# Kernel tuning notes

Hardware: AMD Instinct MI355X
Metric: run time of the kernel (lower is better)

## Reference

```python
import jax, jax.numpy as jnp
import numpy as np

FLOW_W, RECON_W, CONS_W, BIT_W = 1.0, 0.1, 0.1, 0.5
EPS = 1e-7  # guard for log in BCE (torch clamps log at -100)


def setup_inputs() -> dict:
    key = jax.random.key(0)
    k1, k2, k3, k4, k5, k6 = jax.random.split(key, 6)
    B, K, C, T, NB = 8, 4, 2, 262144, 64
    return {
        "separated": jax.random.normal(k1, (B, K, C, T), jnp.float32),
        "sources": jax.random.normal(k2, (B, K, C, T), jnp.float32),
        "mixture": jax.random.normal(k3, (B, C, T), jnp.float32),
        "pred_bits": jax.random.uniform(k4, (B, K, NB), jnp.float32),
        "flow_loss": jax.random.uniform(k5, (1,), jnp.float32),
        "target_bits": jax.random.randint(k6, (B, K, NB), 0, 2, jnp.int32),
    }


def _pit_loss(pred, target):
    # pred/target: [B, K, C, T]; K > 2 path: per-batch KxK MSE cost + greedy matching
    B, K, C, T = pred.shape
    n = C * T
    # cost[b,i,j] = mean((pred[b,i]-target[b,j])^2) expanded to avoid [B,K,K,C,T] intermediate
    p2 = jnp.mean(pred * pred, axis=(-2, -1))            # [B, K]
    t2 = jnp.mean(target * target, axis=(-2, -1))        # [B, K]
    cross = jnp.einsum("bict,bjct->bij", pred, target) / n  # [B, K, K]
    cost = p2[:, :, None] + t2[:, None, :] - 2.0 * cross  # [B, K, K]

    def greedy(c):  # c: [K, K] -> scalar greedy assignment cost
        used = jnp.zeros((K,), bool)
        tot = jnp.zeros((), c.dtype)
        for i in range(K):  # K is small and static
            row = jnp.where(used, jnp.inf, c[i])
            j = jnp.argmin(row)
            tot = tot + row[j]
            used = used.at[j].set(True)
        return tot

    return jnp.mean(jax.vmap(greedy)(cost))  # average over batch


def reference(separated, sources, mixture, pred_bits, flow_loss, target_bits):
    flow = flow_loss[0] * FLOW_W
    recon = _pit_loss(separated, sources) * RECON_W
    mix_hat = separated.sum(axis=1)  # [B, C, T]
    cons = jnp.mean((mix_hat - mixture) ** 2) * CONS_W
    tb = target_bits.astype(pred_bits.dtype)
    p = jnp.clip(pred_bits, EPS, 1.0 - EPS)
    bce = -jnp.mean(tb * jnp.log(p) + (1.0 - tb) * jnp.log(1.0 - p))
    bit = bce * BIT_W
    total = flow + recon + cons + bit
    # [flow_loss, reconstruction_loss, consistency_loss, bit_loss, total_loss]
    return jnp.stack([flow, recon, cons, bit, total])
```

## Files before the change

kernel.cpp:

```cpp
#include <hip/hip_runtime.h>
#include <math.h>

#define BB 8
#define KK 4
#define CT 524288
#define VECS (CT/4)
#define GX 256
#define TPB 256
#define NBITS 2048
#define NACC 25

__global__ __launch_bounds__(256, 4) void floss_reduce(
    const float* __restrict__ sep, const float* __restrict__ src,
    const float* __restrict__ mix, float* __restrict__ ws) {
  const int b = blockIdx.y;
  const float4* sepb = (const float4*)(sep + (size_t)b * KK * CT);
  const float4* srcb = (const float4*)(src + (size_t)b * KK * CT);
  const float4* mixb = (const float4*)(mix + (size_t)b * CT);

  const int v0 = blockIdx.x * (2 * TPB) + threadIdx.x;
  const int v1 = v0 + TPB;

  float4 S0[4], T0[4], S1[4], T1[4], M0, M1;
  #pragma unroll
  for (int k = 0; k < 4; ++k) S0[k] = sepb[(size_t)k * VECS + v0];
  #pragma unroll
  for (int k = 0; k < 4; ++k) T0[k] = srcb[(size_t)k * VECS + v0];
  M0 = mixb[v0];
  #pragma unroll
  for (int k = 0; k < 4; ++k) S1[k] = sepb[(size_t)k * VECS + v1];
  #pragma unroll
  for (int k = 0; k < 4; ++k) T1[k] = srcb[(size_t)k * VECS + v1];
  M1 = mixb[v1];

  float cr[4][4] = {};
  float p2[4] = {};
  float t2[4] = {};
  float cons = 0.f;

  #pragma unroll
  for (int h = 0; h < 2; ++h) {
    const float4* S = h ? S1 : S0;
    const float4* T = h ? T1 : T0;
    const float4  M = h ? M1 : M0;
    float s[4][4], t[4][4], m[4];
    #pragma unroll
    for (int k = 0; k < 4; ++k) {
      s[k][0] = S[k].x; s[k][1] = S[k].y; s[k][2] = S[k].z; s[k][3] = S[k].w;
      t[k][0] = T[k].x; t[k][1] = T[k].y; t[k][2] = T[k].z; t[k][3] = T[k].w;
    }
    m[0] = M.x; m[1] = M.y; m[2] = M.z; m[3] = M.w;
    #pragma unroll
    for (int l = 0; l < 4; ++l) {
      #pragma unroll
      for (int i = 0; i < 4; ++i) {
        p2[i] += s[i][l] * s[i][l];
        t2[i] += t[i][l] * t[i][l];
        #pragma unroll
        for (int j = 0; j < 4; ++j) cr[i][j] += s[i][l] * t[j][l];
      }
      float sm = s[0][l] + s[1][l] + s[2][l] + s[3][l] - m[l];
      cons += sm * sm;
    }
  }

  float acc[NACC];
  #pragma unroll
  for (int i = 0; i < 4; ++i)
    #pragma unroll
    for (int j = 0; j < 4; ++j) acc[i * 4 + j] = cr[i][j];
  #pragma unroll
  for (int i = 0; i < 4; ++i) { acc[16 + i] = p2[i]; acc[20 + i] = t2[i]; }
  acc[24] = cons;

  #pragma unroll
  for (int a = 0; a < NACC; ++a) {
    #pragma unroll
    for (int off = 32; off > 0; off >>= 1)
      acc[a] += __shfl_down(acc[a], off);
  }

  __shared__ float lds[4][NACC];
  const int wave = threadIdx.x >> 6, lane = threadIdx.x & 63;
  if (lane == 0) {
    #pragma unroll
    for (int a = 0; a < NACC; ++a) lds[wave][a] = acc[a];
  }
  __syncthreads();
  if (threadIdx.x < NACC) {
    float v = lds[0][threadIdx.x] + lds[1][threadIdx.x] +
              lds[2][threadIdx.x] + lds[3][threadIdx.x];
    ws[((size_t)threadIdx.x * BB + b) * GX + blockIdx.x] = v;
  }
}

__global__ __launch_bounds__(256) void floss_finalize(
    const float* __restrict__ ws, const float* __restrict__ pred_bits,
    const int* __restrict__ target_bits, const float* __restrict__ flow_loss,
    float* __restrict__ out) {
  __shared__ float sums[BB * NACC];
  const int t = threadIdx.x;

  if (t < BB * NACC) {
    const int a = t >> 3, b = t & 7;
    const float4* p = (const float4*)(ws + ((size_t)a * BB + b) * GX);
    float4 s4 = make_float4(0.f, 0.f, 0.f, 0.f);
    #pragma unroll 8
    for (int g = 0; g < GX / 4; ++g) {
      float4 x = p[g];
      s4.x += x.x; s4.y += x.y; s4.z += x.z; s4.w += x.w;
    }
    sums[b * NACC + a] = s4.x + s4.y + s4.z + s4.w;
  }

  float acc = 0.f;
  for (int i = t; i < NBITS; i += 256) {
    float tb = (float)target_bits[i];
    float p = pred_bits[i];
    p = fminf(fmaxf(p, 1e-7f), 1.f - 1e-7f);
    acc += tb * logf(p) + (1.f - tb) * logf(1.f - p);
  }
  #pragma unroll
  for (int off = 32; off > 0; off >>= 1) acc += __shfl_down(acc, off);
  __shared__ float sacc[4];
  const int wave = t >> 6, lane = t & 63;
  if (lane == 0) sacc[wave] = acc;
  __syncthreads();

  if (t == 0) {
    float bsum = sacc[0] + sacc[1] + sacc[2] + sacc[3];
    float bce = -bsum / (float)NBITS;
    float bit = bce * 0.5f;

    const float inv_n = 1.f / (float)CT;
    float recon_sum = 0.f;
    float cons_sum = 0.f;
    for (int b = 0; b < BB; ++b) {
      const float* w = sums + b * NACC;
      cons_sum += w[24];
      float cost[4][4];
      for (int i = 0; i < 4; ++i)
        for (int j = 0; j < 4; ++j)
          cost[i][j] = (w[16 + i] + w[20 + j] - 2.f * w[i * 4 + j]) * inv_n;
      bool used[4] = {false, false, false, false};
      for (int i = 0; i < 4; ++i) {
        int bj = 0; float bv = INFINITY;
        for (int j = 0; j < 4; ++j) {
          if (!used[j] && cost[i][j] < bv) { bv = cost[i][j]; bj = j; }
        }
        recon_sum += bv; used[bj] = true;
      }
    }
    float recon = recon_sum / (float)BB * 0.1f;
    float cons = cons_sum / (float)(BB * CT) * 0.1f;
    float flow = flow_loss[0];
    out[0] = flow;
    out[1] = recon;
    out[2] = cons;
    out[3] = bit;
    out[4] = flow + recon + cons + bit;
  }
}

extern "C" void kernel_launch(void* const* d_in, const int* in_sizes, int n_in,
                              void* d_out, int out_size, void* d_ws, size_t ws_size,
                              hipStream_t stream) {
  const float* sep       = (const float*)d_in[0];
  const float* src       = (const float*)d_in[1];
  const float* mix       = (const float*)d_in[2];
  const float* pred_bits = (const float*)d_in[3];
  const float* flow      = (const float*)d_in[4];
  const int*   tgt_bits  = (const int*)d_in[5];
  float* ws = (float*)d_ws;

  floss_reduce<<<dim3(GX, BB), TPB, 0, stream>>>(sep, src, mix, ws);
  floss_finalize<<<1, TPB, 0, stream>>>(ws, pred_bits, tgt_bits, flow, (float*)d_out);
}
```

Measured before the change: 47.45 us.

## Stream inputs through double-buffered LDS via async global_load_lds per wave

```diff
diff --git a/kernel.cpp b/kernel.cpp
--- a/kernel.cpp
+++ b/kernel.cpp
@@ -5,44 +5,74 @@
 #define KK 4
 #define CT 524288
 #define VECS (CT/4)
-#define GX 256
+#define GX 64
 #define TPB 256
+#define NWAVE 4
+#define NIT 8
 #define NBITS 2048
 #define NACC 25
-
-__global__ __launch_bounds__(256, 4) void floss_reduce(
+#define SLOT 256
+#define BUF (9*SLOT)
+
+typedef __attribute__((address_space(1))) const void GV;
+typedef __attribute__((address_space(3))) void LV;
+
+__device__ __forceinline__ void gl_lds16(const void* g, void* l) {
+  __builtin_amdgcn_global_load_lds((GV*)g, (LV*)l, 16, 0, 0);
+}
+
+__global__ __launch_bounds__(TPB, 2) void floss_reduce(
     const float* __restrict__ sep, const float* __restrict__ src,
     const float* __restrict__ mix, float* __restrict__ ws) {
+  __shared__ float smem[NWAVE * 2 * BUF];
+  __shared__ float redu[NWAVE][NACC];
+
   const int b = blockIdx.y;
-  const float4* sepb = (const float4*)(sep + (size_t)b * KK * CT);
-  const float4* srcb = (const float4*)(src + (size_t)b * KK * CT);
-  const float4* mixb = (const float4*)(mix + (size_t)b * CT);
-
-  const int v0 = blockIdx.x * (2 * TPB) + threadIdx.x;
-  const int v1 = v0 + TPB;
-
-  float4 S0[4], T0[4], S1[4], T1[4], M0, M1;
-  #pragma unroll
-  for (int k = 0; k < 4; ++k) S0[k] = sepb[(size_t)k * VECS + v0];
-  #pragma unroll
-  for (int k = 0; k < 4; ++k) T0[k] = srcb[(size_t)k * VECS + v0];
-  M0 = mixb[v0];
-  #pragma unroll
-  for (int k = 0; k < 4; ++k) S1[k] = sepb[(size_t)k * VECS + v1];
-  #pragma unroll
-  for (int k = 0; k < 4; ++k) T1[k] = srcb[(size_t)k * VECS + v1];
-  M1 = mixb[v1];
+  const int wave = threadIdx.x >> 6, lane = threadIdx.x & 63;
+
+  const float4* sepv = (const float4*)(sep + (size_t)b * KK * CT);
+  const float4* srcv = (const float4*)(src + (size_t)b * KK * CT);
+  const float4* mixv = (const float4*)(mix + (size_t)b * CT);
+
+  const int wbase = (blockIdx.x * NWAVE + wave) * (NIT * 64);
+  float* wsm = smem + wave * (2 * BUF);
 
   float cr[4][4] = {};
   float p2[4] = {};
   float t2[4] = {};
   float cons = 0.f;
 
-  #pragma unroll
-  for (int h = 0; h < 2; ++h) {
-    const float4* S = h ? S1 : S0;
-    const float4* T = h ? T1 : T0;
-    const float4  M = h ? M1 : M0;
+  auto issue = [&](int it) {
+    float* dst = wsm + (it & 1) * BUF;
+    const int v = wbase + it * 64 + lane;
+    #pragma unroll
+    for (int k = 0; k < 4; ++k)
+      gl_lds16(sepv + (size_t)k * VECS + v, dst + k * SLOT);
+    #pragma unroll
+    for (int k = 0; k < 4; ++k)
+      gl_lds16(srcv + (size_t)k * VECS + v, dst + (4 + k) * SLOT);
+    gl_lds16(mixv + v, dst + 8 * SLOT);
+  };
+
+  issue(0);
+  #pragma unroll
+  for (int it = 0; it < NIT; ++it) {
+    if (it + 1 < NIT) issue(it + 1);
+    __builtin_amdgcn_sched_barrier(0);
+    if (it + 1 < NIT)
+      __builtin_amdgcn_s_waitcnt(0x0F79);
+    else
+      __builtin_amdgcn_s_waitcnt(0x0F70);
+    __builtin_amdgcn_sched_barrier(0);
+
+    const float4* buf = (const float4*)(wsm + (it & 1) * BUF);
+    float4 S[4], T[4], M;
+    #pragma unroll
+    for (int k = 0; k < 4; ++k) S[k] = buf[k * 64 + lane];
+    #pragma unroll
+    for (int k = 0; k < 4; ++k) T[k] = buf[(4 + k) * 64 + lane];
+    M = buf[8 * 64 + lane];
+
     float s[4][4], t[4][4], m[4];
     #pragma unroll
     for (int k = 0; k < 4; ++k) {
@@ -62,6 +92,7 @@
       float sm = s[0][l] + s[1][l] + s[2][l] + s[3][l] - m[l];
       cons += sm * sm;
     }
+    __builtin_amdgcn_sched_barrier(0);
   }
 
   float acc[NACC];
@@ -79,17 +110,14 @@
     for (int off = 32; off > 0; off >>= 1)
       acc[a] += __shfl_down(acc[a], off);
   }
-
-  __shared__ float lds[4][NACC];
-  const int wave = threadIdx.x >> 6, lane = threadIdx.x & 63;
   if (lane == 0) {
     #pragma unroll
-    for (int a = 0; a < NACC; ++a) lds[wave][a] = acc[a];
+    for (int a = 0; a < NACC; ++a) redu[wave][a] = acc[a];
   }
   __syncthreads();
   if (threadIdx.x < NACC) {
-    float v = lds[0][threadIdx.x] + lds[1][threadIdx.x] +
-              lds[2][threadIdx.x] + lds[3][threadIdx.x];
+    float v = redu[0][threadIdx.x] + redu[1][threadIdx.x] +
+              redu[2][threadIdx.x] + redu[3][threadIdx.x];
     ws[((size_t)threadIdx.x * BB + b) * GX + blockIdx.x] = v;
   }
 }
@@ -105,7 +133,7 @@
     const int a = t >> 3, b = t & 7;
     const float4* p = (const float4*)(ws + ((size_t)a * BB + b) * GX);
     float4 s4 = make_float4(0.f, 0.f, 0.f, 0.f);
-    #pragma unroll 8
+    #pragma unroll
     for (int g = 0; g < GX / 4; ++g) {
       float4 x = p[g];
       s4.x += x.x; s4.y += x.y; s4.z += x.z; s4.w += x.w;
```

Measured after the change: 41.98 us. 1.13x faster.

## Software-pipeline reduce kernel with inline-asm loads and explicit vmcnt waits

Applied to the files above, without the earlier changes.

```diff
diff --git a/kernel.cpp b/kernel.cpp
--- a/kernel.cpp
+++ b/kernel.cpp
@@ -5,64 +5,93 @@
 #define KK 4
 #define CT 524288
 #define VECS (CT/4)
-#define GX 256
+#define GX 64
 #define TPB 256
+#define NIT 4
 #define NBITS 2048
 #define NACC 25
 
-__global__ __launch_bounds__(256, 4) void floss_reduce(
+typedef float f32x4 __attribute__((ext_vector_type(4)));
+
+#define LOADA(dst, voff, base) \
+  asm volatile("global_load_dwordx4 %0, %1, %2" : "=&v"(dst) : "v"(voff), "s"(base))
+#define LOADB(dst, voff, base) \
+  asm volatile("global_load_dwordx4 %0, %1, %2 offset:2048" : "=&v"(dst) : "v"(voff), "s"(base))
+#define WAITV(n) do { \
+  __builtin_amdgcn_sched_barrier(0); \
+  asm volatile("s_waitcnt vmcnt(" #n ")" ::: "memory"); \
+  __builtin_amdgcn_sched_barrier(0); } while (0)
+
+#define ISSUE(G0, G1, voff) do { \
+  LOADA(G0[0], (voff), b_s0); LOADA(G0[1], (voff), b_s1); \
+  LOADA(G0[2], (voff), b_s2); LOADA(G0[3], (voff), b_s3); \
+  LOADA(G0[4], (voff), b_t0); LOADA(G0[5], (voff), b_t1); \
+  LOADA(G0[6], (voff), b_t2); LOADA(G0[7], (voff), b_t3); \
+  LOADA(G0[8], (voff), b_mm); \
+  LOADB(G1[0], (voff), b_s0); LOADB(G1[1], (voff), b_s1); \
+  LOADB(G1[2], (voff), b_s2); LOADB(G1[3], (voff), b_s3); \
+  LOADB(G1[4], (voff), b_t0); LOADB(G1[5], (voff), b_t1); \
+  LOADB(G1[6], (voff), b_t2); LOADB(G1[7], (voff), b_t3); \
+  LOADB(G1[8], (voff), b_mm); \
+} while (0)
+
+__global__ __launch_bounds__(TPB, 2) void floss_reduce(
     const float* __restrict__ sep, const float* __restrict__ src,
     const float* __restrict__ mix, float* __restrict__ ws) {
   const int b = blockIdx.y;
-  const float4* sepb = (const float4*)(sep + (size_t)b * KK * CT);
-  const float4* srcb = (const float4*)(src + (size_t)b * KK * CT);
-  const float4* mixb = (const float4*)(mix + (size_t)b * CT);
-
-  const int v0 = blockIdx.x * (2 * TPB) + threadIdx.x;
-  const int v1 = v0 + TPB;
-
-  float4 S0[4], T0[4], S1[4], T1[4], M0, M1;
-  #pragma unroll
-  for (int k = 0; k < 4; ++k) S0[k] = sepb[(size_t)k * VECS + v0];
-  #pragma unroll
-  for (int k = 0; k < 4; ++k) T0[k] = srcb[(size_t)k * VECS + v0];
-  M0 = mixb[v0];
-  #pragma unroll
-  for (int k = 0; k < 4; ++k) S1[k] = sepb[(size_t)k * VECS + v1];
-  #pragma unroll
-  for (int k = 0; k < 4; ++k) T1[k] = srcb[(size_t)k * VECS + v1];
-  M1 = mixb[v1];
+  const float* sepb = sep + (size_t)b * KK * CT;
+  const float* srcb = src + (size_t)b * KK * CT;
+  const float* mixb = mix + (size_t)b * CT;
+
+  const float* b_s0 = sepb + 0 * (size_t)CT;
+  const float* b_s1 = sepb + 1 * (size_t)CT;
+  const float* b_s2 = sepb + 2 * (size_t)CT;
+  const float* b_s3 = sepb + 3 * (size_t)CT;
+  const float* b_t0 = srcb + 0 * (size_t)CT;
+  const float* b_t1 = srcb + 1 * (size_t)CT;
+  const float* b_t2 = srcb + 2 * (size_t)CT;
+  const float* b_t3 = srcb + 3 * (size_t)CT;
+  const float* b_mm = mixb;
+
+  const int tid = threadIdx.x;
+  const int lanepos = ((tid & 128) << 1) + (tid & 127);
+  const unsigned vb = (unsigned)(blockIdx.x * (NIT * 512) + lanepos) * 16u;
 
   float cr[4][4] = {};
   float p2[4] = {};
   float t2[4] = {};
   float cons = 0.f;
 
-  #pragma unroll
-  for (int h = 0; h < 2; ++h) {
-    const float4* S = h ? S1 : S0;
-    const float4* T = h ? T1 : T0;
-    const float4  M = h ? M1 : M0;
-    float s[4][4], t[4][4], m[4];
-    #pragma unroll
-    for (int k = 0; k < 4; ++k) {
-      s[k][0] = S[k].x; s[k][1] = S[k].y; s[k][2] = S[k].z; s[k][3] = S[k].w;
-      t[k][0] = T[k].x; t[k][1] = T[k].y; t[k][2] = T[k].z; t[k][3] = T[k].w;
-    }
-    m[0] = M.x; m[1] = M.y; m[2] = M.z; m[3] = M.w;
+  auto consume = [&](const f32x4 (&D)[9]) {
     #pragma unroll
     for (int l = 0; l < 4; ++l) {
       #pragma unroll
       for (int i = 0; i < 4; ++i) {
-        p2[i] += s[i][l] * s[i][l];
-        t2[i] += t[i][l] * t[i][l];
+        float si = D[i][l], ti = D[4 + i][l];
+        p2[i] += si * si;
+        t2[i] += ti * ti;
         #pragma unroll
-        for (int j = 0; j < 4; ++j) cr[i][j] += s[i][l] * t[j][l];
+        for (int j = 0; j < 4; ++j) cr[i][j] += si * D[4 + j][l];
       }
-      float sm = s[0][l] + s[1][l] + s[2][l] + s[3][l] - m[l];
+      float sm = D[0][l] + D[1][l] + D[2][l] + D[3][l] - D[8][l];
       cons += sm * sm;
     }
-  }
+  };
+
+  f32x4 P0[9], P1[9], Q0[9], Q1[9];
+
+  ISSUE(P0, P1, vb);
+  ISSUE(Q0, Q1, vb + 8192u);
+  WAITV(27); consume(P0);
+  WAITV(18); consume(P1);
+  ISSUE(P0, P1, vb + 16384u);
+  WAITV(27); consume(Q0);
+  WAITV(18); consume(Q1);
+  ISSUE(Q0, Q1, vb + 24576u);
+  WAITV(27); consume(P0);
+  WAITV(18); consume(P1);
+  WAITV(9);  consume(Q0);
+  WAITV(0);  consume(Q1);
 
   float acc[NACC];
   #pragma unroll
@@ -80,17 +109,16 @@
       acc[a] += __shfl_down(acc[a], off);
   }
 
-  __shared__ float lds[4][NACC];
-  const int wave = threadIdx.x >> 6, lane = threadIdx.x & 63;
+  __shared__ float redu[4][NACC];
+  const int wave = tid >> 6, lane = tid & 63;
   if (lane == 0) {
     #pragma unroll
-    for (int a = 0; a < NACC; ++a) lds[wave][a] = acc[a];
+    for (int a = 0; a < NACC; ++a) redu[wave][a] = acc[a];
   }
   __syncthreads();
-  if (threadIdx.x < NACC) {
-    float v = lds[0][threadIdx.x] + lds[1][threadIdx.x] +
-              lds[2][threadIdx.x] + lds[3][threadIdx.x];
-    ws[((size_t)threadIdx.x * BB + b) * GX + blockIdx.x] = v;
+  if (tid < NACC) {
+    float v = redu[0][tid] + redu[1][tid] + redu[2][tid] + redu[3][tid];
+    ws[((size_t)tid * BB + b) * GX + blockIdx.x] = v;
   }
 }
 
@@ -105,7 +133,7 @@
     const int a = t >> 3, b = t & 7;
     const float4* p = (const float4*)(ws + ((size_t)a * BB + b) * GX);
     float4 s4 = make_float4(0.f, 0.f, 0.f, 0.f);
-    #pragma unroll 8
+    #pragma unroll
     for (int g = 0; g < GX / 4; ++g) {
       float4 x = p[g];
       s4.x += x.x; s4.y += x.y; s4.z += x.z; s4.w += x.w;
```

Measured after the change: 43.51 us. 8.3% less time.

## Stream inputs through double-buffered LDS with direct global-to-LDS loads

Applied to the files above, without the earlier changes.

```diff
diff --git a/kernel.cpp b/kernel.cpp
--- a/kernel.cpp
+++ b/kernel.cpp
@@ -4,64 +4,88 @@
 #define BB 8
 #define KK 4
 #define CT 524288
-#define VECS (CT/4)
-#define GX 256
-#define TPB 256
+#define PB (CT/4)
+#define GXB 32
+#define NT 8
+#define TILE 512
+#define TPB 512
 #define NBITS 2048
 #define NACC 25
 
-__global__ __launch_bounds__(256, 4) void floss_reduce(
+typedef float f32x4 __attribute__((ext_vector_type(4)));
+typedef __attribute__((address_space(1))) const void GV;
+typedef __attribute__((address_space(3))) void LV;
+
+__device__ __forceinline__ void gl_lds16(const void* g, void* l) {
+  __builtin_amdgcn_global_load_lds((GV*)g, (LV*)l, 16, 0, 0);
+}
+
+__global__ __launch_bounds__(TPB, 1) void floss_reduce(
     const float* __restrict__ sep, const float* __restrict__ src,
     const float* __restrict__ mix, float* __restrict__ ws) {
+  __shared__ float smem[2][9][TILE * 4];
+  __shared__ float redu[8][NACC];
+
   const int b = blockIdx.y;
-  const float4* sepb = (const float4*)(sep + (size_t)b * KK * CT);
-  const float4* srcb = (const float4*)(src + (size_t)b * KK * CT);
-  const float4* mixb = (const float4*)(mix + (size_t)b * CT);
-
-  const int v0 = blockIdx.x * (2 * TPB) + threadIdx.x;
-  const int v1 = v0 + TPB;
-
-  float4 S0[4], T0[4], S1[4], T1[4], M0, M1;
-  #pragma unroll
-  for (int k = 0; k < 4; ++k) S0[k] = sepb[(size_t)k * VECS + v0];
-  #pragma unroll
-  for (int k = 0; k < 4; ++k) T0[k] = srcb[(size_t)k * VECS + v0];
-  M0 = mixb[v0];
-  #pragma unroll
-  for (int k = 0; k < 4; ++k) S1[k] = sepb[(size_t)k * VECS + v1];
-  #pragma unroll
-  for (int k = 0; k < 4; ++k) T1[k] = srcb[(size_t)k * VECS + v1];
-  M1 = mixb[v1];
+  const int tid  = threadIdx.x;
+  const int wave = tid >> 6, lane = tid & 63;
+
+  const float* sepb = sep + (size_t)b * KK * CT;
+  const float* srcb = src + (size_t)b * KK * CT;
+  const float* mixb = mix + (size_t)b * CT;
+  const float* mybase = (wave < 4) ? (sepb + (size_t)wave * CT)
+                                   : (srcb + (size_t)(wave - 4) * CT);
+
+  const int tile0 = blockIdx.x * NT;
+
+  auto stage = [&](int t, int c) {
+    const size_t pbyte = (size_t)(tile0 + t) * TILE * 16;
+    const char* gsrc = (const char*)mybase + pbyte + (size_t)lane * 16;
+    float* ldst = &smem[c][wave][0];
+    #pragma unroll
+    for (int r = 0; r < 8; ++r)
+      gl_lds16(gsrc + (size_t)r * 1024, ldst + r * 256);
+    const char* gmix = (const char*)mixb + pbyte + (size_t)wave * 1024 + (size_t)lane * 16;
+    gl_lds16(gmix, &smem[c][8][wave * 256]);
+  };
 
   float cr[4][4] = {};
   float p2[4] = {};
   float t2[4] = {};
   float cons = 0.f;
 
-  #pragma unroll
-  for (int h = 0; h < 2; ++h) {
-    const float4* S = h ? S1 : S0;
-    const float4* T = h ? T1 : T0;
-    const float4  M = h ? M1 : M0;
-    float s[4][4], t[4][4], m[4];
-    #pragma unroll
-    for (int k = 0; k < 4; ++k) {
-      s[k][0] = S[k].x; s[k][1] = S[k].y; s[k][2] = S[k].z; s[k][3] = S[k].w;
-      t[k][0] = T[k].x; t[k][1] = T[k].y; t[k][2] = T[k].z; t[k][3] = T[k].w;
-    }
-    m[0] = M.x; m[1] = M.y; m[2] = M.z; m[3] = M.w;
+  stage(0, 0);
+  for (int t = 0; t < NT; ++t) {
+    const int c = t & 1;
+    if (t + 1 < NT) {
+      stage(t + 1, c ^ 1);
+      __builtin_amdgcn_sched_barrier(0);
+      asm volatile("s_waitcnt vmcnt(9)" ::: "memory");
+    } else {
+      __builtin_amdgcn_sched_barrier(0);
+      asm volatile("s_waitcnt vmcnt(0)" ::: "memory");
+    }
+    __syncthreads();
+
+    f32x4 D[9];
+    #pragma unroll
+    for (int s = 0; s < 9; ++s)
+      D[s] = *(const f32x4*)&smem[c][s][tid * 4];
+
     #pragma unroll
     for (int l = 0; l < 4; ++l) {
       #pragma unroll
       for (int i = 0; i < 4; ++i) {
-        p2[i] += s[i][l] * s[i][l];
-        t2[i] += t[i][l] * t[i][l];
+        float si = D[i][l], ti = D[4 + i][l];
+        p2[i] += si * si;
+        t2[i] += ti * ti;
         #pragma unroll
-        for (int j = 0; j < 4; ++j) cr[i][j] += s[i][l] * t[j][l];
+        for (int j = 0; j < 4; ++j) cr[i][j] += si * D[4 + j][l];
       }
-      float sm = s[0][l] + s[1][l] + s[2][l] + s[3][l] - m[l];
+      float sm = D[0][l] + D[1][l] + D[2][l] + D[3][l] - D[8][l];
       cons += sm * sm;
     }
+    __syncthreads();
   }
 
   float acc[NACC];
@@ -79,18 +103,16 @@
     for (int off = 32; off > 0; off >>= 1)
       acc[a] += __shfl_down(acc[a], off);
   }
-
-  __shared__ float lds[4][NACC];
-  const int wave = threadIdx.x >> 6, lane = threadIdx.x & 63;
   if (lane == 0) {
     #pragma unroll
-    for (int a = 0; a < NACC; ++a) lds[wave][a] = acc[a];
+    for (int a = 0; a < NACC; ++a) redu[wave][a] = acc[a];
   }
   __syncthreads();
-  if (threadIdx.x < NACC) {
-    float v = lds[0][threadIdx.x] + lds[1][threadIdx.x] +
-              lds[2][threadIdx.x] + lds[3][threadIdx.x];
-    ws[((size_t)threadIdx.x * BB + b) * GX + blockIdx.x] = v;
+  if (tid < NACC) {
+    float v = 0.f;
+    #pragma unroll
+    for (int w = 0; w < 8; ++w) v += redu[w][tid];
+    ws[((size_t)tid * BB + b) * GXB + blockIdx.x] = v;
   }
 }
 
@@ -103,10 +125,10 @@
 
   if (t < BB * NACC) {
     const int a = t >> 3, b = t & 7;
-    const float4* p = (const float4*)(ws + ((size_t)a * BB + b) * GX);
+    const float4* p = (const float4*)(ws + ((size_t)a * BB + b) * GXB);
     float4 s4 = make_float4(0.f, 0.f, 0.f, 0.f);
-    #pragma unroll 8
-    for (int g = 0; g < GX / 4; ++g) {
+    #pragma unroll
+    for (int g = 0; g < GXB / 4; ++g) {
       float4 x = p[g];
       s4.x += x.x; s4.y += x.y; s4.z += x.z; s4.w += x.w;
     }
@@ -173,6 +195,6 @@
   const int*   tgt_bits  = (const int*)d_in[5];
   float* ws = (float*)d_ws;
 
-  floss_reduce<<<dim3(GX, BB), TPB, 0, stream>>>(sep, src, mix, ws);
-  floss_finalize<<<1, TPB, 0, stream>>>(ws, pred_bits, tgt_bits, flow, (float*)d_out);
-}
+  floss_reduce<<<dim3(GXB, BB), TPB, 0, stream>>>(sep, src, mix, ws);
+  floss_finalize<<<1, 256, 0, stream>>>(ws, pred_bits, tgt_bits, flow, (float*)d_out);
+}
```

Result: faster. 41.72 us (-12.1%).
